# Kernel tuning notes

Measured on AMD Instinct MI355X. Metric: run time of the kernel, lower is better.

Reference implementation:

```python
import jax, jax.numpy as jnp
import numpy as np

NEG = -1000000000.0

def setup_inputs() -> dict:
    key = jax.random.key(0)
    k1, k2, k3, k4 = jax.random.split(key, 4)
    B, T, D, V = 64, 512, 768, 20
    embeddings = jax.random.normal(k1, (B, T, D), dtype=jnp.float32)
    embeddings_mask = jax.random.randint(k2, (B, T), 0, 2, dtype=jnp.int32)
    value_mask = jax.random.randint(k3, (B, V), 0, 2, dtype=jnp.int32)
    value_weight = jax.random.normal(k4, (V, D), dtype=jnp.float32)
    return {"embeddings": embeddings, "embeddings_mask": embeddings_mask,
            "value_mask": value_mask, "value_weight": value_weight}

def reference(embeddings, embeddings_mask, value_mask, value_weight):
    # value attention: scores[b,t,v] = <emb[b,t], W[v]>  (torch does bcast-mul-sum)
    emb_mask = embeddings_mask.astype(jnp.float32)          # (B,T)
    scores = jnp.einsum('btd,vd->btv', embeddings, value_weight)
    scores = scores * emb_mask[:, :, None]                   # mask tokens
    value_scores = scores.sum(axis=1)                        # (B,V)
    value_scores = value_scores + (1.0 - value_mask.astype(jnp.float32)) * NEG
    value_probs = jax.nn.softmax(value_scores, axis=-1)      # (B,V)
    value_embedding = jnp.einsum('bv,vd->bd', value_probs, value_weight)
    # attention pooling over tokens using value_embedding as query
    pooling_scores = jnp.einsum('btd,bd->bt', embeddings, value_embedding)
    pooling_scores = pooling_scores + (1.0 - emb_mask) * NEG
    pooling_probs = jax.nn.softmax(pooling_scores, axis=-1)  # (B,T)
    pooled_embedding = jnp.einsum('btd,bt->bd', embeddings, pooling_probs)
    return (value_embedding, pooled_embedding, value_probs, pooling_probs)
```

## Files before the change

kernel.cpp:

```cpp
#include <hip/hip_runtime.h>
#include <math.h>

#define B 64
#define T 512
#define D 768
#define D4 192
#define V 20
#define NEG -1000000000.0f
#define TCH 32
#define NCH 16
#define NBLK (B * NCH)

__global__ __launch_bounds__(256) void k_sum_vdots(
    const float4* __restrict__ emb4, const int* __restrict__ emask,
    const float* __restrict__ W, float* __restrict__ pd) {
  const int bc = blockIdx.x, b = bc >> 4, c = bc & 15;
  const int tid = threadIdx.x, wave = tid >> 6, lane = tid & 63;
  __shared__ int sm[TCH];
  __shared__ int idx[TCH];
  __shared__ int scnt;
  __shared__ float4 lacc4[4][D4];
  __shared__ float msum[D];

  if (tid < TCH) sm[tid] = emask[b * T + c * TCH + tid];
  __syncthreads();
  if (tid == 0) {
    int n = 0;
    for (int t = 0; t < TCH; ++t)
      if (sm[t]) idx[n++] = t;
    scnt = n;
  }
  __syncthreads();
  const int cnt = scnt;
  const float4* eb = emb4 + ((size_t)b * T + (size_t)c * TCH) * D4;

  float4 s0 = {0.f, 0.f, 0.f, 0.f}, s1 = s0, s2 = s0;
  int i = wave;
  for (; i + 4 < cnt; i += 8) {
    const float4* ea = eb + (size_t)idx[i] * D4 + lane;
    const float4* ec = eb + (size_t)idx[i + 4] * D4 + lane;
    float4 a0 = ea[0], a1 = ea[64], a2 = ea[128];
    float4 b0 = ec[0], b1 = ec[64], b2 = ec[128];
    s0.x += a0.x + b0.x; s0.y += a0.y + b0.y;
    s0.z += a0.z + b0.z; s0.w += a0.w + b0.w;
    s1.x += a1.x + b1.x; s1.y += a1.y + b1.y;
    s1.z += a1.z + b1.z; s1.w += a1.w + b1.w;
    s2.x += a2.x + b2.x; s2.y += a2.y + b2.y;
    s2.z += a2.z + b2.z; s2.w += a2.w + b2.w;
  }
  if (i < cnt) {
    const float4* ea = eb + (size_t)idx[i] * D4 + lane;
    float4 a0 = ea[0], a1 = ea[64], a2 = ea[128];
    s0.x += a0.x; s0.y += a0.y; s0.z += a0.z; s0.w += a0.w;
    s1.x += a1.x; s1.y += a1.y; s1.z += a1.z; s1.w += a1.w;
    s2.x += a2.x; s2.y += a2.y; s2.z += a2.z; s2.w += a2.w;
  }
  lacc4[wave][lane] = s0;
  lacc4[wave][lane + 64] = s1;
  lacc4[wave][lane + 128] = s2;
  __syncthreads();
  if (tid < D4) {
    float4 a = lacc4[0][tid], x = lacc4[1][tid], y = lacc4[2][tid],
           z = lacc4[3][tid];
    float4 r;
    r.x = a.x + x.x + y.x + z.x;
    r.y = a.y + x.y + y.y + z.y;
    r.z = a.z + x.z + y.z + z.z;
    r.w = a.w + x.w + y.w + z.w;
    *(float4*)&msum[4 * tid] = r;
  }
  __syncthreads();
  for (int v = wave; v < V; v += 4) {
    float p = 0.f;
    const float* wv = W + (size_t)v * D;
    for (int j = 0; j < 12; ++j) {
      int d = lane + 64 * j;
      p += msum[d] * wv[d];
    }
    for (int off = 32; off; off >>= 1) p += __shfl_xor(p, off, 64);
    if (lane == 0) pd[bc * V + v] = p;
  }
}

__global__ __launch_bounds__(256) void k_fused_pool(
    const float4* __restrict__ emb4, const int* __restrict__ emask,
    const int* __restrict__ vmask, const float* __restrict__ W,
    const float* __restrict__ pd, float* __restrict__ vemb_out,
    float* __restrict__ vprobs_out, float* __restrict__ scores,
    float* __restrict__ pm, float* __restrict__ pl,
    float4* __restrict__ pacc4) {
  const int bc = blockIdx.x, b = bc >> 4, c = bc & 15;
  const int tid = threadIdx.x, wave = tid >> 6, lane = tid & 63;
  __shared__ int sm[TCH];
  __shared__ int idx[TCH];
  __shared__ int scnt;
  __shared__ float4 lacc4[4][D4];
  __shared__ float vemb[D];
  __shared__ float sc[V], pr[V];
  __shared__ float lm[4], ll[4], co4[4];

  if (tid < TCH) sm[tid] = emask[b * T + c * TCH + tid];
  __syncthreads();
  if (tid == 0) {
    int n = 0;
    for (int t = 0; t < TCH; ++t)
      if (sm[t]) idx[n++] = t;
    scnt = n;
  }

  if (tid < V) {
    float s = 0.f;
    for (int cc = 0; cc < NCH; ++cc) s += pd[(b * NCH + cc) * V + tid];
    sc[tid] = s + (vmask[b * V + tid] ? 0.f : NEG);
  }
  __syncthreads();
  if (tid == 0) {
    float m = sc[0];
    for (int v = 1; v < V; ++v) m = fmaxf(m, sc[v]);
    float ssum = 0.f;
    for (int v = 0; v < V; ++v) {
      float e = expf(sc[v] - m);
      pr[v] = e;
      ssum += e;
    }
    float inv = 1.f / ssum;
    for (int v = 0; v < V; ++v) {
      pr[v] *= inv;
      if (c == 0) vprobs_out[b * V + v] = pr[v];
    }
  }
  __syncthreads();
  for (int k = 0; k < 3; ++k) {
    int d = tid + 256 * k;
    float a = 0.f;
    for (int v = 0; v < V; ++v) a += pr[v] * W[(size_t)v * D + d];
    vemb[d] = a;
    if (c == 0) vemb_out[(size_t)b * D + d] = a;
  }
  __syncthreads();

  const int cnt = scnt;
  const float4* eb = emb4 + ((size_t)b * T + (size_t)c * TCH) * D4;
  const float4* vb = (const float4*)vemb;
  float4 ve0 = vb[lane], ve1 = vb[lane + 64], ve2 = vb[lane + 128];
  float* srow = scores + b * T + c * TCH;
  float m = NEG, l = 0.f;
  float4 a0 = {0.f, 0.f, 0.f, 0.f}, a1 = a0, a2 = a0;
  int i = wave;
  for (; i + 4 < cnt; i += 8) {
    int t0 = idx[i], t1 = idx[i + 4];
    const float4* ea = eb + (size_t)t0 * D4 + lane;
    const float4* ec = eb + (size_t)t1 * D4 + lane;
    float4 e0 = ea[0], e1 = ea[64], e2 = ea[128];
    float4 f0 = ec[0], f1 = ec[64], f2 = ec[128];
    float p0 = e0.x * ve0.x + e0.y * ve0.y + e0.z * ve0.z + e0.w * ve0.w +
               e1.x * ve1.x + e1.y * ve1.y + e1.z * ve1.z + e1.w * ve1.w +
               e2.x * ve2.x + e2.y * ve2.y + e2.z * ve2.z + e2.w * ve2.w;
    float p1 = f0.x * ve0.x + f0.y * ve0.y + f0.z * ve0.z + f0.w * ve0.w +
               f1.x * ve1.x + f1.y * ve1.y + f1.z * ve1.z + f1.w * ve1.w +
               f2.x * ve2.x + f2.y * ve2.y + f2.z * ve2.z + f2.w * ve2.w;
    for (int off = 32; off; off >>= 1) {
      p0 += __shfl_xor(p0, off, 64);
      p1 += __shfl_xor(p1, off, 64);
    }
    if (lane == 0) { srow[t0] = p0; srow[t1] = p1; }
    float mn = fmaxf(m, fmaxf(p0, p1));
    float scale = expf(m - mn);
    float w0 = expf(p0 - mn), w1 = expf(p1 - mn);
    l = l * scale + w0 + w1;
    a0.x = a0.x * scale + w0 * e0.x + w1 * f0.x;
    a0.y = a0.y * scale + w0 * e0.y + w1 * f0.y;
    a0.z = a0.z * scale + w0 * e0.z + w1 * f0.z;
    a0.w = a0.w * scale + w0 * e0.w + w1 * f0.w;
    a1.x = a1.x * scale + w0 * e1.x + w1 * f1.x;
    a1.y = a1.y * scale + w0 * e1.y + w1 * f1.y;
    a1.z = a1.z * scale + w0 * e1.z + w1 * f1.z;
    a1.w = a1.w * scale + w0 * e1.w + w1 * f1.w;
    a2.x = a2.x * scale + w0 * e2.x + w1 * f2.x;
    a2.y = a2.y * scale + w0 * e2.y + w1 * f2.y;
    a2.z = a2.z * scale + w0 * e2.z + w1 * f2.z;
    a2.w = a2.w * scale + w0 * e2.w + w1 * f2.w;
    m = mn;
  }
  if (i < cnt) {
    int t0 = idx[i];
    const float4* ea = eb + (size_t)t0 * D4 + lane;
    float4 e0 = ea[0], e1 = ea[64], e2 = ea[128];
    float p0 = e0.x * ve0.x + e0.y * ve0.y + e0.z * ve0.z + e0.w * ve0.w +
               e1.x * ve1.x + e1.y * ve1.y + e1.z * ve1.z + e1.w * ve1.w +
               e2.x * ve2.x + e2.y * ve2.y + e2.z * ve2.z + e2.w * ve2.w;
    for (int off = 32; off; off >>= 1) p0 += __shfl_xor(p0, off, 64);
    if (lane == 0) srow[t0] = p0;
    float mn = fmaxf(m, p0);
    float scale = expf(m - mn);
    float w0 = expf(p0 - mn);
    l = l * scale + w0;
    a0.x = a0.x * scale + w0 * e0.x; a0.y = a0.y * scale + w0 * e0.y;
    a0.z = a0.z * scale + w0 * e0.z; a0.w = a0.w * scale + w0 * e0.w;
    a1.x = a1.x * scale + w0 * e1.x; a1.y = a1.y * scale + w0 * e1.y;
    a1.z = a1.z * scale + w0 * e1.z; a1.w = a1.w * scale + w0 * e1.w;
    a2.x = a2.x * scale + w0 * e2.x; a2.y = a2.y * scale + w0 * e2.y;
    a2.z = a2.z * scale + w0 * e2.z; a2.w = a2.w * scale + w0 * e2.w;
    m = mn;
  }
  if (lane == 0) { lm[wave] = m; ll[wave] = l; }
  lacc4[wave][lane] = a0;
  lacc4[wave][lane + 64] = a1;
  lacc4[wave][lane + 128] = a2;
  __syncthreads();
  if (tid == 0) {
    float M = fmaxf(fmaxf(lm[0], lm[1]), fmaxf(lm[2], lm[3]));
    float L = 0.f;
    for (int w2 = 0; w2 < 4; ++w2) {
      float cw = expf(lm[w2] - M);
      co4[w2] = cw;
      L += ll[w2] * cw;
    }
    pm[bc] = M;
    pl[bc] = L;
  }
  __syncthreads();
  if (tid < D4) {
    float4 r = {0.f, 0.f, 0.f, 0.f};
    for (int w2 = 0; w2 < 4; ++w2) {
      float cw = co4[w2];
      float4 a = lacc4[w2][tid];
      r.x += cw * a.x; r.y += cw * a.y;
      r.z += cw * a.z; r.w += cw * a.w;
    }
    pacc4[(size_t)bc * D4 + tid] = r;
  }
}

__global__ __launch_bounds__(256) void k_finalize(
    const float* __restrict__ pm, const float* __restrict__ pl,
    const float4* __restrict__ pacc4, const float* __restrict__ scores,
    const int* __restrict__ emask, float* __restrict__ pooled,
    float* __restrict__ pprobs) {
  const int b = blockIdx.x, tid = threadIdx.x;
  __shared__ float co[NCH];
  __shared__ float sM, sinvL;
  if (tid == 0) {
    float M = NEG;
    for (int cc = 0; cc < NCH; ++cc) M = fmaxf(M, pm[b * NCH + cc]);
    float L = 0.f;
    for (int cc = 0; cc < NCH; ++cc)
      L += pl[b * NCH + cc] * expf(pm[b * NCH + cc] - M);
    float invL = 1.f / L;
    for (int cc = 0; cc < NCH; ++cc)
      co[cc] = expf(pm[b * NCH + cc] - M) * invL;
    sM = M;
    sinvL = invL;
  }
  __syncthreads();
  if (tid < D4) {
    float4 r = {0.f, 0.f, 0.f, 0.f};
    for (int cc = 0; cc < NCH; ++cc) {
      float cw = co[cc];
      float4 a = pacc4[(size_t)(b * NCH + cc) * D4 + tid];
      r.x += cw * a.x; r.y += cw * a.y;
      r.z += cw * a.z; r.w += cw * a.w;
    }
    ((float4*)pooled)[(size_t)b * D4 + tid] = r;
  }
  float M = sM, invL = sinvL;
  for (int k = 0; k < 2; ++k) {
    int t = tid + 256 * k;
    pprobs[b * T + t] =
        emask[b * T + t] ? expf(scores[b * T + t] - M) * invL : 0.f;
  }
}

extern "C" void kernel_launch(void* const* d_in, const int* in_sizes, int n_in,
                              void* d_out, int out_size, void* d_ws,
                              size_t ws_size, hipStream_t stream) {
  const float4* emb4 = (const float4*)d_in[0];
  const int* emask = (const int*)d_in[1];
  const int* vmask = (const int*)d_in[2];
  const float* W = (const float*)d_in[3];

  float* out = (float*)d_out;
  float* vemb_out = out;
  float* pooled_out = out + B * D;
  float* vprobs_out = out + 2 * B * D;
  float* pprobs_out = out + 2 * B * D + B * V;

  float* ws = (float*)d_ws;
  float* pacc = ws;
  float* scores = pacc + NBLK * D;
  float* pm = scores + B * T;
  float* pl = pm + NBLK;
  float* pd = pl + NBLK;

  k_sum_vdots<<<dim3(NBLK), dim3(256), 0, stream>>>(emb4, emask, W, pd);
  k_fused_pool<<<dim3(NBLK), dim3(256), 0, stream>>>(
      emb4, emask, vmask, W, pd, vemb_out, vprobs_out, scores, pm, pl,
      (float4*)pacc);
  k_finalize<<<dim3(B), dim3(256), 0, stream>>>(pm, pl, (const float4*)pacc,
                                                scores, emask, pooled_out,
                                                pprobs_out);
}
```

Measured before the change: 165.6 us.

## Fuse three kernels into one using per-batch atomic barrier and last-block finalize

Merges the vdot-sum, fused pooling and finalize kernels into a single kernel. A per-batch atomic counter with a spin-wait acts as a grid barrier between the value-score stage and the pooling stage. A last-arriving-block counter lets one block per batch do the final cross-chunk softmax merge. This removes two kernel launches and their boundaries, and the second pass over each embedding chunk happens soon after the first, which may improve cache reuse. The spin barrier assumes all 1024 blocks are resident at once, so it risks deadlock if occupancy is lower than expected. It also adds a memset to clear the counters.

```diff
diff --git a/kernel.cpp b/kernel.cpp
--- a/kernel.cpp
+++ b/kernel.cpp
@@ -11,16 +11,29 @@
 #define NCH 16
 #define NBLK (B * NCH)
 
-__global__ __launch_bounds__(256) void k_sum_vdots(
+__global__ __launch_bounds__(256, 4) void k_all(
     const float4* __restrict__ emb4, const int* __restrict__ emask,
-    const float* __restrict__ W, float* __restrict__ pd) {
+    const int* __restrict__ vmask, const float* __restrict__ W,
+    float* __restrict__ vemb_out, float* __restrict__ pooled_out,
+    float* __restrict__ vprobs_out, float* __restrict__ pprobs_out,
+    float* __restrict__ ws, unsigned* __restrict__ cntA,
+    unsigned* __restrict__ cntC) {
   const int bc = blockIdx.x, b = bc >> 4, c = bc & 15;
   const int tid = threadIdx.x, wave = tid >> 6, lane = tid & 63;
-  __shared__ int sm[TCH];
-  __shared__ int idx[TCH];
-  __shared__ int scnt;
+
+  float* pacc = ws;
+  float* scores = pacc + NBLK * D;
+  float* pm = scores + B * T;
+  float* pl = pm + NBLK;
+  float* pd = pl + NBLK;
+
+  __shared__ int sm[TCH], idx[TCH], scnt;
   __shared__ float4 lacc4[4][D4];
-  __shared__ float msum[D];
+  __shared__ float buf[D];
+  __shared__ float sc[V], pr[V];
+  __shared__ float lm[4], ll[4], co4[4], coS[NCH];
+  __shared__ float sM, sinvL;
+  __shared__ int amLast;
 
   if (tid < TCH) sm[tid] = emask[b * T + c * TCH + tid];
   __syncthreads();
@@ -34,79 +47,65 @@
   const int cnt = scnt;
   const float4* eb = emb4 + ((size_t)b * T + (size_t)c * TCH) * D4;
 
-  float4 s0 = {0.f, 0.f, 0.f, 0.f}, s1 = s0, s2 = s0;
-  int i = wave;
-  for (; i + 4 < cnt; i += 8) {
-    const float4* ea = eb + (size_t)idx[i] * D4 + lane;
-    const float4* ec = eb + (size_t)idx[i + 4] * D4 + lane;
-    float4 a0 = ea[0], a1 = ea[64], a2 = ea[128];
-    float4 b0 = ec[0], b1 = ec[64], b2 = ec[128];
-    s0.x += a0.x + b0.x; s0.y += a0.y + b0.y;
-    s0.z += a0.z + b0.z; s0.w += a0.w + b0.w;
-    s1.x += a1.x + b1.x; s1.y += a1.y + b1.y;
-    s1.z += a1.z + b1.z; s1.w += a1.w + b1.w;
-    s2.x += a2.x + b2.x; s2.y += a2.y + b2.y;
-    s2.z += a2.z + b2.z; s2.w += a2.w + b2.w;
-  }
-  if (i < cnt) {
-    const float4* ea = eb + (size_t)idx[i] * D4 + lane;
-    float4 a0 = ea[0], a1 = ea[64], a2 = ea[128];
-    s0.x += a0.x; s0.y += a0.y; s0.z += a0.z; s0.w += a0.w;
-    s1.x += a1.x; s1.y += a1.y; s1.z += a1.z; s1.w += a1.w;
-    s2.x += a2.x; s2.y += a2.y; s2.z += a2.z; s2.w += a2.w;
-  }
-  lacc4[wave][lane] = s0;
-  lacc4[wave][lane + 64] = s1;
-  lacc4[wave][lane + 128] = s2;
-  __syncthreads();
-  if (tid < D4) {
-    float4 a = lacc4[0][tid], x = lacc4[1][tid], y = lacc4[2][tid],
-           z = lacc4[3][tid];
-    float4 r;
-    r.x = a.x + x.x + y.x + z.x;
-    r.y = a.y + x.y + y.y + z.y;
-    r.z = a.z + x.z + y.z + z.z;
-    r.w = a.w + x.w + y.w + z.w;
-    *(float4*)&msum[4 * tid] = r;
-  }
-  __syncthreads();
-  for (int v = wave; v < V; v += 4) {
-    float p = 0.f;
-    const float* wv = W + (size_t)v * D;
-    for (int j = 0; j < 12; ++j) {
-      int d = lane + 64 * j;
-      p += msum[d] * wv[d];
-    }
-    for (int off = 32; off; off >>= 1) p += __shfl_xor(p, off, 64);
-    if (lane == 0) pd[bc * V + v] = p;
-  }
-}
-
-__global__ __launch_bounds__(256) void k_fused_pool(
-    const float4* __restrict__ emb4, const int* __restrict__ emask,
-    const int* __restrict__ vmask, const float* __restrict__ W,
-    const float* __restrict__ pd, float* __restrict__ vemb_out,
-    float* __restrict__ vprobs_out, float* __restrict__ scores,
-    float* __restrict__ pm, float* __restrict__ pl,
-    float4* __restrict__ pacc4) {
-  const int bc = blockIdx.x, b = bc >> 4, c = bc & 15;
-  const int tid = threadIdx.x, wave = tid >> 6, lane = tid & 63;
-  __shared__ int sm[TCH];
-  __shared__ int idx[TCH];
-  __shared__ int scnt;
-  __shared__ float4 lacc4[4][D4];
-  __shared__ float vemb[D];
-  __shared__ float sc[V], pr[V];
-  __shared__ float lm[4], ll[4], co4[4];
-
-  if (tid < TCH) sm[tid] = emask[b * T + c * TCH + tid];
-  __syncthreads();
-  if (tid == 0) {
-    int n = 0;
-    for (int t = 0; t < TCH; ++t)
-      if (sm[t]) idx[n++] = t;
-    scnt = n;
-  }
+  {
+    float4 s0 = {0.f, 0.f, 0.f, 0.f}, s1 = s0, s2 = s0;
+    int i = wave;
+    for (; i + 4 < cnt; i += 8) {
+      const float4* ea = eb + (size_t)idx[i] * D4 + lane;
+      const float4* ec = eb + (size_t)idx[i + 4] * D4 + lane;
+      float4 a0 = ea[0], a1 = ea[64], a2 = ea[128];
+      float4 b0 = ec[0], b1 = ec[64], b2 = ec[128];
+      s0.x += a0.x + b0.x; s0.y += a0.y + b0.y;
+      s0.z += a0.z + b0.z; s0.w += a0.w + b0.w;
+      s1.x += a1.x + b1.x; s1.y += a1.y + b1.y;
+      s1.z += a1.z + b1.z; s1.w += a1.w + b1.w;
+      s2.x += a2.x + b2.x; s2.y += a2.y + b2.y;
+      s2.z += a2.z + b2.z; s2.w += a2.w + b2.w;
+    }
+    if (i < cnt) {
+      const float4* ea = eb + (size_t)idx[i] * D4 + lane;
+      float4 a0 = ea[0], a1 = ea[64], a2 = ea[128];
+      s0.x += a0.x; s0.y += a0.y; s0.z += a0.z; s0.w += a0.w;
+      s1.x += a1.x; s1.y += a1.y; s1.z += a1.z; s1.w += a1.w;
+      s2.x += a2.x; s2.y += a2.y; s2.z += a2.z; s2.w += a2.w;
+    }
+    lacc4[wave][lane] = s0;
+    lacc4[wave][lane + 64] = s1;
+    lacc4[wave][lane + 128] = s2;
+    __syncthreads();
+    if (tid < D4) {
+      float4 a = lacc4[0][tid], x = lacc4[1][tid], y = lacc4[2][tid],
+             z = lacc4[3][tid];
+      float4 r;
+      r.x = a.x + x.x + y.x + z.x;
+      r.y = a.y + x.y + y.y + z.y;
+      r.z = a.z + x.z + y.z + z.z;
+      r.w = a.w + x.w + y.w + z.w;
+      *(float4*)&buf[4 * tid] = r;
+    }
+    __syncthreads();
+    for (int v = wave; v < V; v += 4) {
+      float p = 0.f;
+      const float* wv = W + (size_t)v * D;
+      for (int j = 0; j < 12; ++j) {
+        int d = lane + 64 * j;
+        p += buf[d] * wv[d];
+      }
+      for (int off = 32; off; off >>= 1) p += __shfl_xor(p, off, 64);
+      if (lane == 0) pd[bc * V + v] = p;
+    }
+  }
+
+  __syncthreads();
+  if (tid == 0) {
+    __threadfence();
+    atomicAdd(&cntA[b], 1u);
+    while (__hip_atomic_load(&cntA[b], __ATOMIC_RELAXED,
+                             __HIP_MEMORY_SCOPE_AGENT) < (unsigned)NCH)
+      __builtin_amdgcn_s_sleep(8);
+    __threadfence();
+  }
+  __syncthreads();
 
   if (tid < V) {
     float s = 0.f;
@@ -134,140 +133,142 @@
     int d = tid + 256 * k;
     float a = 0.f;
     for (int v = 0; v < V; ++v) a += pr[v] * W[(size_t)v * D + d];
-    vemb[d] = a;
+    buf[d] = a;
     if (c == 0) vemb_out[(size_t)b * D + d] = a;
   }
   __syncthreads();
 
-  const int cnt = scnt;
-  const float4* eb = emb4 + ((size_t)b * T + (size_t)c * TCH) * D4;
-  const float4* vb = (const float4*)vemb;
-  float4 ve0 = vb[lane], ve1 = vb[lane + 64], ve2 = vb[lane + 128];
-  float* srow = scores + b * T + c * TCH;
-  float m = NEG, l = 0.f;
-  float4 a0 = {0.f, 0.f, 0.f, 0.f}, a1 = a0, a2 = a0;
-  int i = wave;
-  for (; i + 4 < cnt; i += 8) {
-    int t0 = idx[i], t1 = idx[i + 4];
-    const float4* ea = eb + (size_t)t0 * D4 + lane;
-    const float4* ec = eb + (size_t)t1 * D4 + lane;
-    float4 e0 = ea[0], e1 = ea[64], e2 = ea[128];
-    float4 f0 = ec[0], f1 = ec[64], f2 = ec[128];
-    float p0 = e0.x * ve0.x + e0.y * ve0.y + e0.z * ve0.z + e0.w * ve0.w +
-               e1.x * ve1.x + e1.y * ve1.y + e1.z * ve1.z + e1.w * ve1.w +
-               e2.x * ve2.x + e2.y * ve2.y + e2.z * ve2.z + e2.w * ve2.w;
-    float p1 = f0.x * ve0.x + f0.y * ve0.y + f0.z * ve0.z + f0.w * ve0.w +
-               f1.x * ve1.x + f1.y * ve1.y + f1.z * ve1.z + f1.w * ve1.w +
-               f2.x * ve2.x + f2.y * ve2.y + f2.z * ve2.z + f2.w * ve2.w;
-    for (int off = 32; off; off >>= 1) {
-      p0 += __shfl_xor(p0, off, 64);
-      p1 += __shfl_xor(p1, off, 64);
-    }
-    if (lane == 0) { srow[t0] = p0; srow[t1] = p1; }
-    float mn = fmaxf(m, fmaxf(p0, p1));
-    float scale = expf(m - mn);
-    float w0 = expf(p0 - mn), w1 = expf(p1 - mn);
-    l = l * scale + w0 + w1;
-    a0.x = a0.x * scale + w0 * e0.x + w1 * f0.x;
-    a0.y = a0.y * scale + w0 * e0.y + w1 * f0.y;
-    a0.z = a0.z * scale + w0 * e0.z + w1 * f0.z;
-    a0.w = a0.w * scale + w0 * e0.w + w1 * f0.w;
-    a1.x = a1.x * scale + w0 * e1.x + w1 * f1.x;
-    a1.y = a1.y * scale + w0 * e1.y + w1 * f1.y;
-    a1.z = a1.z * scale + w0 * e1.z + w1 * f1.z;
-    a1.w = a1.w * scale + w0 * e1.w + w1 * f1.w;
-    a2.x = a2.x * scale + w0 * e2.x + w1 * f2.x;
-    a2.y = a2.y * scale + w0 * e2.y + w1 * f2.y;
-    a2.z = a2.z * scale + w0 * e2.z + w1 * f2.z;
-    a2.w = a2.w * scale + w0 * e2.w + w1 * f2.w;
-    m = mn;
-  }
-  if (i < cnt) {
-    int t0 = idx[i];
-    const float4* ea = eb + (size_t)t0 * D4 + lane;
-    float4 e0 = ea[0], e1 = ea[64], e2 = ea[128];
-    float p0 = e0.x * ve0.x + e0.y * ve0.y + e0.z * ve0.z + e0.w * ve0.w +
-               e1.x * ve1.x + e1.y * ve1.y + e1.z * ve1.z + e1.w * ve1.w +
-               e2.x * ve2.x + e2.y * ve2.y + e2.z * ve2.z + e2.w * ve2.w;
-    for (int off = 32; off; off >>= 1) p0 += __shfl_xor(p0, off, 64);
-    if (lane == 0) srow[t0] = p0;
-    float mn = fmaxf(m, p0);
-    float scale = expf(m - mn);
-    float w0 = expf(p0 - mn);
-    l = l * scale + w0;
-    a0.x = a0.x * scale + w0 * e0.x; a0.y = a0.y * scale + w0 * e0.y;
-    a0.z = a0.z * scale + w0 * e0.z; a0.w = a0.w * scale + w0 * e0.w;
-    a1.x = a1.x * scale + w0 * e1.x; a1.y = a1.y * scale + w0 * e1.y;
-    a1.z = a1.z * scale + w0 * e1.z; a1.w = a1.w * scale + w0 * e1.w;
-    a2.x = a2.x * scale + w0 * e2.x; a2.y = a2.y * scale + w0 * e2.y;
-    a2.z = a2.z * scale + w0 * e2.z; a2.w = a2.w * scale + w0 * e2.w;
-    m = mn;
-  }
-  if (lane == 0) { lm[wave] = m; ll[wave] = l; }
-  lacc4[wave][lane] = a0;
-  lacc4[wave][lane + 64] = a1;
-  lacc4[wave][lane + 128] = a2;
-  __syncthreads();
-  if (tid == 0) {
-    float M = fmaxf(fmaxf(lm[0], lm[1]), fmaxf(lm[2], lm[3]));
-    float L = 0.f;
-    for (int w2 = 0; w2 < 4; ++w2) {
-      float cw = expf(lm[w2] - M);
-      co4[w2] = cw;
-      L += ll[w2] * cw;
-    }
-    pm[bc] = M;
-    pl[bc] = L;
-  }
-  __syncthreads();
-  if (tid < D4) {
-    float4 r = {0.f, 0.f, 0.f, 0.f};
-    for (int w2 = 0; w2 < 4; ++w2) {
-      float cw = co4[w2];
-      float4 a = lacc4[w2][tid];
-      r.x += cw * a.x; r.y += cw * a.y;
-      r.z += cw * a.z; r.w += cw * a.w;
-    }
-    pacc4[(size_t)bc * D4 + tid] = r;
-  }
-}
-
-__global__ __launch_bounds__(256) void k_finalize(
-    const float* __restrict__ pm, const float* __restrict__ pl,
-    const float4* __restrict__ pacc4, const float* __restrict__ scores,
-    const int* __restrict__ emask, float* __restrict__ pooled,
-    float* __restrict__ pprobs) {
-  const int b = blockIdx.x, tid = threadIdx.x;
-  __shared__ float co[NCH];
-  __shared__ float sM, sinvL;
-  if (tid == 0) {
-    float M = NEG;
-    for (int cc = 0; cc < NCH; ++cc) M = fmaxf(M, pm[b * NCH + cc]);
-    float L = 0.f;
-    for (int cc = 0; cc < NCH; ++cc)
-      L += pl[b * NCH + cc] * expf(pm[b * NCH + cc] - M);
-    float invL = 1.f / L;
-    for (int cc = 0; cc < NCH; ++cc)
-      co[cc] = expf(pm[b * NCH + cc] - M) * invL;
-    sM = M;
-    sinvL = invL;
-  }
-  __syncthreads();
-  if (tid < D4) {
-    float4 r = {0.f, 0.f, 0.f, 0.f};
-    for (int cc = 0; cc < NCH; ++cc) {
-      float cw = co[cc];
-      float4 a = pacc4[(size_t)(b * NCH + cc) * D4 + tid];
-      r.x += cw * a.x; r.y += cw * a.y;
-      r.z += cw * a.z; r.w += cw * a.w;
-    }
-    ((float4*)pooled)[(size_t)b * D4 + tid] = r;
-  }
-  float M = sM, invL = sinvL;
-  for (int k = 0; k < 2; ++k) {
-    int t = tid + 256 * k;
-    pprobs[b * T + t] =
-        emask[b * T + t] ? expf(scores[b * T + t] - M) * invL : 0.f;
+  {
+    const float4* vb = (const float4*)buf;
+    float4 ve0 = vb[lane], ve1 = vb[lane + 64], ve2 = vb[lane + 128];
+    float* srow = scores + b * T + c * TCH;
+    float m = NEG, l = 0.f;
+    float4 a0 = {0.f, 0.f, 0.f, 0.f}, a1 = a0, a2 = a0;
+    int i = wave;
+    for (; i + 4 < cnt; i += 8) {
+      int t0 = idx[i], t1 = idx[i + 4];
+      const float4* ea = eb + (size_t)t0 * D4 + lane;
+      const float4* ec = eb + (size_t)t1 * D4 + lane;
+      float4 e0 = ea[0], e1 = ea[64], e2 = ea[128];
+      float4 f0 = ec[0], f1 = ec[64], f2 = ec[128];
+      float p0 = e0.x * ve0.x + e0.y * ve0.y + e0.z * ve0.z + e0.w * ve0.w +
+                 e1.x * ve1.x + e1.y * ve1.y + e1.z * ve1.z + e1.w * ve1.w +
+                 e2.x * ve2.x + e2.y * ve2.y + e2.z * ve2.z + e2.w * ve2.w;
+      float p1 = f0.x * ve0.x + f0.y * ve0.y + f0.z * ve0.z + f0.w * ve0.w +
+                 f1.x * ve1.x + f1.y * ve1.y + f1.z * ve1.z + f1.w * ve1.w +
+                 f2.x * ve2.x + f2.y * ve2.y + f2.z * ve2.z + f2.w * ve2.w;
+      for (int off = 32; off; off >>= 1) {
+        p0 += __shfl_xor(p0, off, 64);
+        p1 += __shfl_xor(p1, off, 64);
+      }
+      if (lane == 0) { srow[t0] = p0; srow[t1] = p1; }
+      float mn = fmaxf(m, fmaxf(p0, p1));
+      float scale = expf(m - mn);
+      float w0 = expf(p0 - mn), w1 = expf(p1 - mn);
+      l = l * scale + w0 + w1;
+      a0.x = a0.x * scale + w0 * e0.x + w1 * f0.x;
+      a0.y = a0.y * scale + w0 * e0.y + w1 * f0.y;
+      a0.z = a0.z * scale + w0 * e0.z + w1 * f0.z;
+      a0.w = a0.w * scale + w0 * e0.w + w1 * f0.w;
+      a1.x = a1.x * scale + w0 * e1.x + w1 * f1.x;
+      a1.y = a1.y * scale + w0 * e1.y + w1 * f1.y;
+      a1.z = a1.z * scale + w0 * e1.z + w1 * f1.z;
+      a1.w = a1.w * scale + w0 * e1.w + w1 * f1.w;
+      a2.x = a2.x * scale + w0 * e2.x + w1 * f2.x;
+      a2.y = a2.y * scale + w0 * e2.y + w1 * f2.y;
+      a2.z = a2.z * scale + w0 * e2.z + w1 * f2.z;
+      a2.w = a2.w * scale + w0 * e2.w + w1 * f2.w;
+      m = mn;
+    }
+    if (i < cnt) {
+      int t0 = idx[i];
+      const float4* ea = eb + (size_t)t0 * D4 + lane;
+      float4 e0 = ea[0], e1 = ea[64], e2 = ea[128];
+      float p0 = e0.x * ve0.x + e0.y * ve0.y + e0.z * ve0.z + e0.w * ve0.w +
+                 e1.x * ve1.x + e1.y * ve1.y + e1.z * ve1.z + e1.w * ve1.w +
+                 e2.x * ve2.x + e2.y * ve2.y + e2.z * ve2.z + e2.w * ve2.w;
+      for (int off = 32; off; off >>= 1) p0 += __shfl_xor(p0, off, 64);
+      if (lane == 0) srow[t0] = p0;
+      float mn = fmaxf(m, p0);
+      float scale = expf(m - mn);
+      float w0 = expf(p0 - mn);
+      l = l * scale + w0;
+      a0.x = a0.x * scale + w0 * e0.x; a0.y = a0.y * scale + w0 * e0.y;
+      a0.z = a0.z * scale + w0 * e0.z; a0.w = a0.w * scale + w0 * e0.w;
+      a1.x = a1.x * scale + w0 * e1.x; a1.y = a1.y * scale + w0 * e1.y;
+      a1.z = a1.z * scale + w0 * e1.z; a1.w = a1.w * scale + w0 * e1.w;
+      a2.x = a2.x * scale + w0 * e2.x; a2.y = a2.y * scale + w0 * e2.y;
+      a2.z = a2.z * scale + w0 * e2.z; a2.w = a2.w * scale + w0 * e2.w;
+      m = mn;
+    }
+    if (lane == 0) { lm[wave] = m; ll[wave] = l; }
+    lacc4[wave][lane] = a0;
+    lacc4[wave][lane + 64] = a1;
+    lacc4[wave][lane + 128] = a2;
+    __syncthreads();
+    if (tid == 0) {
+      float M = fmaxf(fmaxf(lm[0], lm[1]), fmaxf(lm[2], lm[3]));
+      float L = 0.f;
+      for (int w2 = 0; w2 < 4; ++w2) {
+        float cw = expf(lm[w2] - M);
+        co4[w2] = cw;
+        L += ll[w2] * cw;
+      }
+      pm[bc] = M;
+      pl[bc] = L;
+    }
+    __syncthreads();
+    if (tid < D4) {
+      float4 r = {0.f, 0.f, 0.f, 0.f};
+      for (int w2 = 0; w2 < 4; ++w2) {
+        float cw = co4[w2];
+        float4 a = lacc4[w2][tid];
+        r.x += cw * a.x; r.y += cw * a.y;
+        r.z += cw * a.z; r.w += cw * a.w;
+      }
+      ((float4*)pacc)[(size_t)bc * D4 + tid] = r;
+    }
+  }
+
+  __syncthreads();
+  if (tid == 0) {
+    __threadfence();
+    unsigned prev = atomicAdd(&cntC[b], 1u);
+    amLast = (prev == (unsigned)(NCH - 1)) ? 1 : 0;
+    if (amLast) __threadfence();
+  }
+  __syncthreads();
+
+  if (amLast) {
+    if (tid == 0) {
+      float M = NEG;
+      for (int cc = 0; cc < NCH; ++cc) M = fmaxf(M, pm[b * NCH + cc]);
+      float L = 0.f;
+      for (int cc = 0; cc < NCH; ++cc)
+        L += pl[b * NCH + cc] * expf(pm[b * NCH + cc] - M);
+      float invL = 1.f / L;
+      for (int cc = 0; cc < NCH; ++cc)
+        coS[cc] = expf(pm[b * NCH + cc] - M) * invL;
+      sM = M;
+      sinvL = invL;
+    }
+    __syncthreads();
+    if (tid < D4) {
+      float4 r = {0.f, 0.f, 0.f, 0.f};
+      for (int cc = 0; cc < NCH; ++cc) {
+        float cw = coS[cc];
+        float4 a = ((const float4*)pacc)[(size_t)(b * NCH + cc) * D4 + tid];
+        r.x += cw * a.x; r.y += cw * a.y;
+        r.z += cw * a.z; r.w += cw * a.w;
+      }
+      ((float4*)pooled_out)[(size_t)b * D4 + tid] = r;
+    }
+    float M = sM, invL = sinvL;
+    for (int k = 0; k < 2; ++k) {
+      int t = tid + 256 * k;
+      pprobs_out[b * T + t] =
+          emask[b * T + t] ? expf(scores[b * T + t] - M) * invL : 0.f;
+    }
   }
 }
 
@@ -286,17 +287,12 @@
   float* pprobs_out = out + 2 * B * D + B * V;
 
   float* ws = (float*)d_ws;
-  float* pacc = ws;
-  float* scores = pacc + NBLK * D;
-  float* pm = scores + B * T;
-  float* pl = pm + NBLK;
-  float* pd = pl + NBLK;
-
-  k_sum_vdots<<<dim3(NBLK), dim3(256), 0, stream>>>(emb4, emask, W, pd);
-  k_fused_pool<<<dim3(NBLK), dim3(256), 0, stream>>>(
-      emb4, emask, vmask, W, pd, vemb_out, vprobs_out, scores, pm, pl,
-      (float4*)pacc);
-  k_finalize<<<dim3(B), dim3(256), 0, stream>>>(pm, pl, (const float4*)pacc,
-                                                scores, emask, pooled_out,
-                                                pprobs_out);
+  size_t ws_floats = (size_t)NBLK * D + B * T + 2 * NBLK + (size_t)NBLK * V;
+  unsigned* cntA = (unsigned*)(ws + ws_floats);
+  unsigned* cntC = cntA + B;
+
+  hipMemsetAsync(cntA, 0, 2 * B * sizeof(unsigned), stream);
+  k_all<<<dim3(NBLK), dim3(256), 0, stream>>>(emb4, emask, vmask, W, vemb_out,
+                                              pooled_out, vprobs_out,
+                                              pprobs_out, ws, cntA, cntC);
 }
```

After: 293.3 us. 77.2% more time.
